# Optimization experiments

Hardware: AMD Instinct MI355X
Metric: run time of the kernel (lower is better)

## Reference

```python
import jax, jax.numpy as jnp
import numpy as np

TH, TL = 0.85, 0.5          # sim thresholds
ALPHA = 0.1                 # proto EMA alpha
TEMP = 1.0                  # readout temperature
KEEP, REFINE, REPLACE, SPAWN = 0, 1, 2, 3


def _l2n(x, axis=-1):
    return x / jnp.maximum(jnp.linalg.norm(x, axis=axis, keepdims=True), 1e-12)


def setup_inputs() -> dict:
    key = jax.random.key(0)
    ks = jax.random.split(key, 12)
    B, N, C, H, W, K = 4, 8, 256, 64, 64, 16
    return {
        "value_BNCHW": jax.random.normal(ks[0], (B, N, C, H, W), jnp.float32),
        "frame_feat_BCHW": jax.random.normal(ks[1], (B, C, H, W), jnp.float32),
        "mask_BNHW": jax.random.uniform(ks[2], (B, N, H, W), jnp.float32),
        "proto": jax.random.normal(ks[3], (B, N, K, C), jnp.float32),
        "age": jax.random.uniform(ks[4], (B, N, K), jnp.float32) * 10.0,
        "usage": jax.random.uniform(ks[5], (B, N, K), jnp.float32) * 5.0,
        "conf": jax.random.uniform(ks[6], (B, N, K), jnp.float32),
        "valid": jax.random.bernoulli(ks[7], 0.7, (B, N, K)),
        "W1": jax.random.normal(ks[8], (C + K + 3 * K, 256), jnp.float32) * 0.02,
        "b1": jnp.zeros((256,), jnp.float32),
        "W2": jax.random.normal(ks[9], (256, 4), jnp.float32) * 0.02,
        "b2": jnp.zeros((4,), jnp.float32),
        "proto_gate": jnp.float32(1.0),
        "frame_gate": jnp.float32(1.0),
    }


def reference(value_BNCHW, frame_feat_BCHW, mask_BNHW, proto, age, usage, conf,
              valid, W1, b1, W2, b2, proto_gate, frame_gate):
    B, N, C, H, W = value_BNCHW.shape
    K = proto.shape[2]
    P = H * W

    # ---- candidate prototype: masked mean pool over HW ----
    flat_v = value_BNCHW.reshape(B, N, C, P)          # [B,N,C,P]
    flat_m = mask_BNHW.reshape(B, N, 1, P)            # [B,N,1,P]
    denom = flat_m.sum(-1)                            # [B,N,1]
    cand = (flat_v * flat_m).sum(-1) / jnp.maximum(denom, 1e-6)
    fallback = flat_v.mean(-1)
    cand = jnp.where(denom <= 1e-5, fallback, cand)   # [B,N,C]
    mask_strength = flat_m.mean(-1)[..., 0]           # [B,N]
    cand = _l2n(cand)

    # ---- cosine sim against bank + context ----
    norm_bank = _l2n(proto)
    sim = jnp.einsum('bnc,bnkc->bnk', cand, norm_bank)
    sim = jnp.where(valid, sim, -1.0)
    g_t = frame_feat_BCHW.mean((2, 3))                # [B,C]
    age_n = age / jnp.maximum(jax.lax.stop_gradient(age.max()), 1.0)
    use_n = usage / jnp.maximum(jax.lax.stop_gradient(usage.max()), 1.0)
    stats = jnp.stack([age_n, use_n, conf], -1).reshape(B, N, 3 * K)
    context = jnp.concatenate(
        [jnp.broadcast_to(g_t[:, None, :], (B, N, C)), sim, stats], -1)
    any_valid = valid.any(-1)
    target_slot = jnp.where(any_valid, sim.argmax(-1), 0)
    max_sim = jnp.take_along_axis(sim, target_slot[..., None], -1)[..., 0]
    max_sim = jnp.where(any_valid, max_sim, 0.0)

    # ---- policy MLP (logits logged; rule-based policy selects action) ----
    logits = jax.nn.gelu(context @ W1 + b1) @ W2 + b2  # [B,N,4]

    has_free = (~valid).any(-1)
    low = max_sim < TL
    action = jnp.full((B, N), REFINE, jnp.int32)
    action = jnp.where(max_sim > TH, KEEP, action)
    action = jnp.where(low & has_free, SPAWN, action)
    action = jnp.where(low & ~has_free, REPLACE, action)

    # ---- action-conditioned slot selection + scatter update ----
    worst = jnp.argmax(age - usage - conf + 1000.0 * (~valid), -1)
    free_slot = jnp.argmax(~valid, -1)
    spawn = action == SPAWN
    replace = action == REPLACE
    refine = action == REFINE
    keep = action == KEEP
    chosen = target_slot
    chosen = jnp.where(spawn & has_free, free_slot, chosen)
    chosen = jnp.where(spawn & ~has_free, worst, chosen)   # spawn_replace_when_full
    chosen = jnp.where(replace, worst, chosen)
    update = refine | replace | spawn
    replace_like = replace | spawn

    bi = jnp.arange(B)[:, None]
    ni = jnp.arange(N)[None, :]

    old_p = proto[bi, ni, chosen]                      # [B,N,C] gather
    refined = _l2n((1.0 - ALPHA) * old_p + ALPHA * cand)
    new_p = jnp.where(refine[..., None], refined,
                      jnp.where(replace_like[..., None], cand, old_p))
    proto_new = proto.at[bi, ni, chosen].set(new_p)

    age1 = age + 1.0
    age_new = age1.at[bi, ni, chosen].set(
        jnp.where(replace_like, 0.0, age1[bi, ni, chosen]))
    usage_new = usage.at[bi, ni, chosen].set(
        jnp.where(replace_like, 1.0,
                  usage[bi, ni, chosen] + (refine | keep).astype(jnp.float32)))
    conf_g = conf[bi, ni, chosen]
    conf_val = jnp.where(refine, jnp.clip(0.5 * conf_g + 0.5 * max_sim, 0.0, 1.0),
                         jnp.where(replace_like, jnp.clip(mask_strength, 0.0, 1.0),
                                   conf_g))
    conf_new = conf.at[bi, ni, chosen].set(conf_val)
    valid_new = valid.at[bi, ni, chosen].set(valid[bi, ni, chosen] | update)

    # ---- prototype-conditioned readout (softmax over bank slots per pixel) ----
    vn = flat_v / jnp.maximum(jnp.linalg.norm(flat_v, axis=2, keepdims=True), 1e-12)
    nb = _l2n(proto_new)
    scores = jnp.einsum('bnkc,bncp->bnkp', nb, vn) / TEMP
    scores = jnp.where(valid_new[..., None], scores, -1e9)
    wts = jax.nn.softmax(scores, axis=2)               # over K
    proto_map = jnp.einsum('bnkp,bnkc->bncp', wts, proto_new)
    proto_map = jnp.where(valid_new.any(-1)[:, :, None, None], proto_map, 0.0)
    proto_map = proto_map.reshape(B, N, C, H, W)

    conditioned = (value_BNCHW + proto_gate * proto_map
                   + frame_gate * frame_feat_BCHW[:, None])
    return conditioned, logits
```

## Files before the change

### kernel.cpp

```cpp
#include <hip/hip_runtime.h>
#include <math.h>

#define NB_B 4
#define NB_N 8
#define NB_C 256
#define NB_K 16
#define NB_P 4096
#define NB_BN (NB_B * NB_N)

typedef float nfloat4 __attribute__((ext_vector_type(4)));

#define WS_WSUM 0
#define WS_VSUM (NB_BN * NB_C)
#define WS_GT   (2 * NB_BN * NB_C)
#define WS_DEN  (WS_GT + NB_B * NB_C)
#define WS_NB   17440
#define WS_PN   (WS_NB + NB_BN * NB_K * NB_C)
#define WS_VAL  (WS_PN + NB_BN * NB_K * NB_C)

__device__ __forceinline__ float2 blk_sum2(float a, float b, float2* sbuf) {
#pragma unroll
  for (int off = 32; off > 0; off >>= 1) {
    a += __shfl_down(a, off, 64);
    b += __shfl_down(b, off, 64);
  }
  int lane = threadIdx.x & 63, wid = threadIdx.x >> 6;
  __syncthreads();
  if (lane == 0) sbuf[wid] = make_float2(a, b);
  __syncthreads();
  float2 r;
  r.x = sbuf[0].x + sbuf[1].x + sbuf[2].x + sbuf[3].x;
  r.y = sbuf[0].y + sbuf[1].y + sbuf[2].y + sbuf[3].y;
  return r;
}

__device__ __forceinline__ float2 blk_max2(float a, float b, float2* sbuf) {
#pragma unroll
  for (int off = 32; off > 0; off >>= 1) {
    a = fmaxf(a, __shfl_down(a, off, 64));
    b = fmaxf(b, __shfl_down(b, off, 64));
  }
  int lane = threadIdx.x & 63, wid = threadIdx.x >> 6;
  __syncthreads();
  if (lane == 0) sbuf[wid] = make_float2(a, b);
  __syncthreads();
  float2 r;
  r.x = fmaxf(fmaxf(sbuf[0].x, sbuf[1].x), fmaxf(sbuf[2].x, sbuf[3].x));
  r.y = fmaxf(fmaxf(sbuf[0].y, sbuf[1].y), fmaxf(sbuf[2].y, sbuf[3].y));
  return r;
}

__device__ __forceinline__ int validMode(const void* vptr) {
  const unsigned int* w = (const unsigned int*)vptr;
  int mode = 0;
  for (int i = 0; i < 128; ++i) {
    unsigned int x = w[i];
    if (x == 0x3f800000u) return 2;
    if (x > 1u) mode = 1;
  }
  return mode;
}
__device__ __forceinline__ bool getValid(const void* vptr, int mode, int idx) {
  if (mode == 1) return ((const unsigned char*)vptr)[idx] != 0;
  if (mode == 2) return ((const float*)vptr)[idx] != 0.0f;
  return ((const int*)vptr)[idx] != 0;
}

__global__ __launch_bounds__(256) void k1_reduce(
    const float* __restrict__ value, const float* __restrict__ frame,
    const float* __restrict__ mask, float* __restrict__ ws) {
  __shared__ float2 sbuf[4];
  int gid = blockIdx.x, tid = threadIdx.x;
  if (gid < NB_BN * NB_C) {
    int bn = gid >> 8;
    const float4* v4 = (const float4*)(value + (size_t)gid * NB_P);
    const float4* m4 = (const float4*)(mask + (size_t)bn * NB_P);
    float wsum = 0.f, vsum = 0.f;
#pragma unroll
    for (int i = 0; i < NB_P / 4 / 256; ++i) {
      float4 a = v4[i * 256 + tid];
      float4 m = m4[i * 256 + tid];
      wsum += a.x * m.x + a.y * m.y + a.z * m.z + a.w * m.w;
      vsum += a.x + a.y + a.z + a.w;
    }
    float2 r = blk_sum2(wsum, vsum, sbuf);
    if (tid == 0) { ws[WS_WSUM + gid] = r.x; ws[WS_VSUM + gid] = r.y; }
  } else if (gid < NB_BN * NB_C + NB_B * NB_C) {
    int idx = gid - NB_BN * NB_C;
    const float4* f4 = (const float4*)(frame + (size_t)idx * NB_P);
    float s = 0.f;
#pragma unroll
    for (int i = 0; i < 4; ++i) {
      float4 a = f4[i * 256 + tid];
      s += a.x + a.y + a.z + a.w;
    }
    float2 r = blk_sum2(s, 0.f, sbuf);
    if (tid == 0) ws[WS_GT + idx] = r.x * (1.0f / NB_P);
  } else {
    int bn = gid - NB_BN * NB_C - NB_B * NB_C;
    const float4* m4 = (const float4*)(mask + (size_t)bn * NB_P);
    float s = 0.f;
#pragma unroll
    for (int i = 0; i < 4; ++i) {
      float4 a = m4[i * 256 + tid];
      s += a.x + a.y + a.z + a.w;
    }
    float2 r = blk_sum2(s, 0.f, sbuf);
    if (tid == 0) ws[WS_DEN + bn] = r.x;
  }
}

__global__ __launch_bounds__(256) void k2_policy(
    const float* __restrict__ proto, const float* __restrict__ age,
    const float* __restrict__ usage, const float* __restrict__ conf,
    const void* __restrict__ valid, const float* __restrict__ W1,
    const float* __restrict__ b1, const float* __restrict__ W2,
    const float* __restrict__ b2, float* __restrict__ ws,
    float* __restrict__ out_logits) {
  __shared__ float2 sbuf[4];
  __shared__ float s_cand[NB_C];
  __shared__ float s_sim[NB_K];
  __shared__ float s_invn[NB_K];
  __shared__ float s_ctx[NB_C + NB_K + 3 * NB_K];
  __shared__ int s_dec[4];
  __shared__ int s_vmode;

  int bn = blockIdx.x;
  int b = bn >> 3;
  int c = threadIdx.x;
  if (c == 0) s_vmode = validMode(valid);

  float denom = ws[WS_DEN + bn];
  float cand;
  if (denom <= 1e-5f) cand = ws[WS_VSUM + bn * NB_C + c] * (1.0f / NB_P);
  else                cand = ws[WS_WSUM + bn * NB_C + c] / fmaxf(denom, 1e-6f);
  float2 r0 = blk_sum2(cand * cand, 0.f, sbuf);
  cand *= 1.0f / fmaxf(sqrtf(r0.x), 1e-12f);
  s_cand[c] = cand;
  __syncthreads();
  int vmode = s_vmode;

  const float* pr = proto + (size_t)bn * NB_K * NB_C;
  {
    int wid = c >> 6, lane = c & 63;
#pragma unroll
    for (int q = 0; q < 4; ++q) {
      int k = wid * 4 + q;
      float pp = 0.f, pc = 0.f;
#pragma unroll
      for (int t = 0; t < 4; ++t) {
        int cc = lane + t * 64;
        float p = pr[k * NB_C + cc];
        pp += p * p;
        pc += p * s_cand[cc];
      }
#pragma unroll
      for (int off = 32; off > 0; off >>= 1) {
        pp += __shfl_down(pp, off, 64);
        pc += __shfl_down(pc, off, 64);
      }
      if (lane == 0) {
        float invk = 1.0f / fmaxf(sqrtf(pp), 1e-12f);
        s_invn[k] = invk;
        s_sim[k] = getValid(valid, vmode, bn * NB_K + k) ? pc * invk : -1.0f;
      }
    }
  }

  float am = fmaxf(age[c], age[c + 256]);
  float um = fmaxf(usage[c], usage[c + 256]);
  float2 mx = blk_max2(am, um, sbuf);
  float age_max = fmaxf(mx.x, 1.0f);
  float use_max = fmaxf(mx.y, 1.0f);

  s_ctx[c] = ws[WS_GT + b * NB_C + c];
  if (c < NB_K) {
    int k = c;
    s_ctx[NB_C + k] = s_sim[k];
    s_ctx[NB_C + NB_K + 3 * k + 0] = age[bn * NB_K + k] / age_max;
    s_ctx[NB_C + NB_K + 3 * k + 1] = usage[bn * NB_K + k] / use_max;
    s_ctx[NB_C + NB_K + 3 * k + 2] = conf[bn * NB_K + k];
  }
  __syncthreads();

  float acc = b1[c];
  for (int i = 0; i < NB_C + 4 * NB_K; ++i) acc += s_ctx[i] * W1[i * 256 + c];
  float h = 0.5f * acc *
            (1.0f + tanhf(0.7978845608028654f * (acc + 0.044715f * acc * acc * acc)));
  for (int j = 0; j < 4; ++j) {
    float2 lj = blk_sum2(h * W2[c * 4 + j], 0.f, sbuf);
    if (c == 0) out_logits[bn * 4 + j] = lj.x + b2[j];
  }

  if (c == 0) {
    bool anyv = false, hasfree = false;
    for (int k = 0; k < NB_K; ++k) {
      if (getValid(valid, vmode, bn * NB_K + k)) anyv = true; else hasfree = true;
    }
    int tgt = 0; float best = s_sim[0];
    for (int k = 1; k < NB_K; ++k) if (s_sim[k] > best) { best = s_sim[k]; tgt = k; }
    if (!anyv) tgt = 0;
    float max_sim = anyv ? s_sim[tgt] : 0.0f;
    int action = 1;
    if (max_sim > 0.85f) action = 0;
    bool low = max_sim < 0.5f;
    if (low && hasfree) action = 3;
    if (low && !hasfree) action = 2;
    int worst = 0; float wb = -1e30f;
    for (int k = 0; k < NB_K; ++k) {
      float sc = age[bn * NB_K + k] - usage[bn * NB_K + k] - conf[bn * NB_K + k] +
                 (getValid(valid, vmode, bn * NB_K + k) ? 0.f : 1000.f);
      if (sc > wb) { wb = sc; worst = k; }
    }
    int freeslot = 0;
    for (int k = 0; k < NB_K; ++k) {
      if (!getValid(valid, vmode, bn * NB_K + k)) { freeslot = k; break; }
    }
    int chosen = tgt;
    if (action == 3) chosen = hasfree ? freeslot : worst;
    if (action == 2) chosen = worst;
    s_dec[0] = chosen;
    s_dec[1] = (action == 1);
    s_dec[2] = (action == 2 || action == 3);
    s_dec[3] = (action != 0);
  }
  __syncthreads();

  int chosen = s_dec[0];
  float oldp = pr[chosen * NB_C + c];
  float t = 0.9f * oldp + 0.1f * s_cand[c];
  float2 tn = blk_sum2(t * t, 0.f, sbuf);
  float invt = 1.0f / fmaxf(sqrtf(tn.x), 1e-12f);
  float pn_chosen = s_dec[1] ? t * invt : (s_dec[2] ? s_cand[c] : oldp);
  float nb_chosen = s_dec[1] ? t * invt
                   : (s_dec[2] ? s_cand[c] : oldp * s_invn[chosen]);
  float nbrow[NB_K], pnrow[NB_K];
#pragma unroll
  for (int k = 0; k < NB_K; ++k) {
    float praw = pr[k * NB_C + c];
    nbrow[k] = (k == chosen) ? nb_chosen : praw * s_invn[k];
    pnrow[k] = (k == chosen) ? pn_chosen : praw;
  }
  float* nbp = ws + WS_NB + (size_t)bn * NB_K * NB_C + c * NB_K;
  float* pnp = ws + WS_PN + (size_t)bn * NB_K * NB_C + c * NB_K;
#pragma unroll
  for (int q = 0; q < 4; ++q) {
    *(float4*)(nbp + 4 * q) =
        make_float4(nbrow[4 * q], nbrow[4 * q + 1], nbrow[4 * q + 2], nbrow[4 * q + 3]);
    *(float4*)(pnp + 4 * q) =
        make_float4(pnrow[4 * q], pnrow[4 * q + 1], pnrow[4 * q + 2], pnrow[4 * q + 3]);
  }
  if (c < NB_K) {
    bool v = getValid(valid, vmode, bn * NB_K + c) || (c == chosen && s_dec[3]);
    ws[WS_VAL + bn * NB_K + c] = v ? 1.0f : 0.0f;
  }
}

__global__ __launch_bounds__(256, 4) void k3_fused(
    const float* __restrict__ value, const float* __restrict__ frame,
    const float* __restrict__ ws, const float* __restrict__ pgp,
    const float* __restrict__ fgp, float* __restrict__ out) {
  __shared__ float s_nb[NB_C * NB_K];
  __shared__ float4 s_part[4][64][5];
  int blk = blockIdx.x;
  int bn = blk >> 4, pxc = blk & 15;
  int b = bn >> 3;
  int tid = threadIdx.x;
  int lane = tid & 63, wv = tid >> 6;
  int px = pxc * 256 + lane * 4;

  const float4* nb4 = (const float4*)(ws + WS_NB + (size_t)bn * NB_K * NB_C);
  const float4* pn4 = (const float4*)(ws + WS_PN + (size_t)bn * NB_K * NB_C);
  float4* snb4 = (float4*)s_nb;
#pragma unroll
  for (int j = 0; j < 4; ++j) snb4[j * 256 + tid] = nb4[j * 256 + tid];
  int vmask = 0;
  for (int k = 0; k < NB_K; ++k)
    if (ws[WS_VAL + bn * NB_K + k] != 0.0f) vmask |= (1 << k);
  float pg = pgp[0], fg = fgp[0];
  __syncthreads();

  const float* vp = value + (size_t)bn * NB_C * NB_P + px;
  const float* nbk = s_nb + wv * 4;
  float4 dq0 = make_float4(0.f, 0.f, 0.f, 0.f);
  float4 dq1 = dq0, dq2 = dq0, dq3 = dq0, ss = dq0;
#pragma unroll 8
  for (int c = 0; c < NB_C; ++c) {
    float4 v = *(const float4*)(vp + (size_t)c * NB_P);
    float4 nk = *(const float4*)(nbk + c * NB_K);
    ss.x += v.x * v.x; ss.y += v.y * v.y; ss.z += v.z * v.z; ss.w += v.w * v.w;
    dq0.x += v.x * nk.x; dq0.y += v.y * nk.x; dq0.z += v.z * nk.x; dq0.w += v.w * nk.x;
    dq1.x += v.x * nk.y; dq1.y += v.y * nk.y; dq1.z += v.z * nk.y; dq1.w += v.w * nk.y;
    dq2.x += v.x * nk.z; dq2.y += v.y * nk.z; dq2.z += v.z * nk.z; dq2.w += v.w * nk.z;
    dq3.x += v.x * nk.w; dq3.y += v.y * nk.w; dq3.z += v.z * nk.w; dq3.w += v.w * nk.w;
  }

  s_part[wv][lane][0] = dq0;
  s_part[wv][lane][1] = dq1;
  s_part[wv][lane][2] = dq2;
  s_part[wv][lane][3] = dq3;
  __syncthreads();

  float4 d[NB_K];
#pragma unroll
  for (int k = 0; k < NB_K; ++k) d[k] = s_part[k >> 2][lane][k & 3];

#pragma unroll
  for (int j = 0; j < 4; ++j) snb4[j * 256 + tid] = pn4[j * 256 + tid];

  float4 invv;
  invv.x = 1.0f / fmaxf(sqrtf(ss.x), 1e-12f);
  invv.y = 1.0f / fmaxf(sqrtf(ss.y), 1e-12f);
  invv.z = 1.0f / fmaxf(sqrtf(ss.z), 1e-12f);
  invv.w = 1.0f / fmaxf(sqrtf(ss.w), 1e-12f);
  float4 m = make_float4(-1e30f, -1e30f, -1e30f, -1e30f);
#pragma unroll
  for (int k = 0; k < NB_K; ++k) {
    d[k].x *= invv.x; d[k].y *= invv.y; d[k].z *= invv.z; d[k].w *= invv.w;
    if ((vmask >> k) & 1) {
      m.x = fmaxf(m.x, d[k].x); m.y = fmaxf(m.y, d[k].y);
      m.z = fmaxf(m.z, d[k].z); m.w = fmaxf(m.w, d[k].w);
    }
  }
  float4 es = make_float4(0.f, 0.f, 0.f, 0.f);
#pragma unroll
  for (int k = 0; k < NB_K; ++k) {
    if ((vmask >> k) & 1) {
      d[k].x = __expf(d[k].x - m.x); d[k].y = __expf(d[k].y - m.y);
      d[k].z = __expf(d[k].z - m.z); d[k].w = __expf(d[k].w - m.w);
      es.x += d[k].x; es.y += d[k].y; es.z += d[k].z; es.w += d[k].w;
    } else {
      d[k] = make_float4(0.f, 0.f, 0.f, 0.f);
    }
  }
  float4 isum;
  isum.x = vmask ? (1.0f / es.x) : 0.0f;
  isum.y = vmask ? (1.0f / es.y) : 0.0f;
  isum.z = vmask ? (1.0f / es.z) : 0.0f;
  isum.w = vmask ? (1.0f / es.w) : 0.0f;
#pragma unroll
  for (int k = 0; k < NB_K; ++k) {
    d[k].x *= isum.x; d[k].y *= isum.y; d[k].z *= isum.z; d[k].w *= isum.w;
  }
  __syncthreads();

  int c0 = wv * 64;
  const float* vp2 = value + ((size_t)bn * NB_C + c0) * NB_P + px;
  const float* fp = frame + ((size_t)b * NB_C + c0) * NB_P + px;
  float* op = out + ((size_t)bn * NB_C + c0) * NB_P + px;
  const float* spn = s_nb + (size_t)c0 * NB_K;
#pragma unroll 4
  for (int cc = 0; cc < 64; ++cc) {
    float4 v = *(const float4*)(vp2 + (size_t)cc * NB_P);
    float4 f = *(const float4*)(fp + (size_t)cc * NB_P);
    const float4* prow = (const float4*)(spn + cc * NB_K);
    float4 p0 = prow[0], p1 = prow[1], p2 = prow[2], p3 = prow[3];
    float4 pm = make_float4(0.f, 0.f, 0.f, 0.f);
#define APM(K, S)                                                        \
    pm.x += d[K].x * S; pm.y += d[K].y * S; pm.z += d[K].z * S; pm.w += d[K].w * S;
    APM(0, p0.x)  APM(1, p0.y)  APM(2, p0.z)  APM(3, p0.w)
    APM(4, p1.x)  APM(5, p1.y)  APM(6, p1.z)  APM(7, p1.w)
    APM(8, p2.x)  APM(9, p2.y)  APM(10, p2.z) APM(11, p2.w)
    APM(12, p3.x) APM(13, p3.y) APM(14, p3.z) APM(15, p3.w)
#undef APM
    nfloat4 o;
    o.x = v.x + pg * pm.x + fg * f.x;
    o.y = v.y + pg * pm.y + fg * f.y;
    o.z = v.z + pg * pm.z + fg * f.z;
    o.w = v.w + pg * pm.w + fg * f.w;
    __builtin_nontemporal_store(o, (nfloat4*)(op + (size_t)cc * NB_P));
  }
}

extern "C" void kernel_launch(void* const* d_in, const int* in_sizes, int n_in,
                              void* d_out, int out_size, void* d_ws, size_t ws_size,
                              hipStream_t stream) {
  const float* value = (const float*)d_in[0];
  const float* frame = (const float*)d_in[1];
  const float* mask  = (const float*)d_in[2];
  const float* proto = (const float*)d_in[3];
  const float* age   = (const float*)d_in[4];
  const float* usage = (const float*)d_in[5];
  const float* conf  = (const float*)d_in[6];
  const void*  valid = (const void*)d_in[7];
  const float* W1 = (const float*)d_in[8];
  const float* b1 = (const float*)d_in[9];
  const float* W2 = (const float*)d_in[10];
  const float* b2 = (const float*)d_in[11];
  const float* pg = (const float*)d_in[12];
  const float* fg = (const float*)d_in[13];
  float* out = (float*)d_out;
  float* ws = (float*)d_ws;

  int g1 = NB_BN * NB_C + NB_B * NB_C + NB_BN;
  hipLaunchKernelGGL(k1_reduce, dim3(g1), dim3(256), 0, stream,
                     value, frame, mask, ws);
  hipLaunchKernelGGL(k2_policy, dim3(NB_BN), dim3(256), 0, stream,
                     proto, age, usage, conf, valid, W1, b1, W2, b2, ws,
                     out + (size_t)NB_BN * NB_C * NB_P);
  hipLaunchKernelGGL(k3_fused, dim3(NB_BN * 16), dim3(256), 0, stream,
                     value, frame, ws, pg, fg, out);
}
```

Before: 129.1 us.

## Stage value tiles into LDS with async double-buffered loads shared across waves

In the fused readout kernel's score phase, every wave used to load all 256 channel rows of value for the same pixels, so each row was fetched from global memory four times. Each wave now copies a quarter of each 16-channel chunk straight into LDS with global_load_lds, double-buffered so the next chunk loads while the current one is computed. The per-wave partial dot products are exchanged through a new LDS array, the pn bank is prefetched into registers before the barrier, and one barrier is removed. In exchange, LDS use grows to roughly 65 KB per block and the min-blocks launch bound is dropped, which may lower occupancy and adds a barrier per chunk.

```diff
diff --git a/kernel.cpp b/kernel.cpp
--- a/kernel.cpp
+++ b/kernel.cpp
@@ -17,6 +17,12 @@
 #define WS_NB   17440
 #define WS_PN   (WS_NB + NB_BN * NB_K * NB_C)
 #define WS_VAL  (WS_PN + NB_BN * NB_K * NB_C)
+
+__device__ __forceinline__ void stage16(const float* g, float* l) {
+  __builtin_amdgcn_global_load_lds(
+      (const __attribute__((address_space(1))) unsigned int*)g,
+      (__attribute__((address_space(3))) unsigned int*)l, 16, 0, 0);
+}
 
 __device__ __forceinline__ float2 blk_sum2(float a, float b, float2* sbuf) {
 #pragma unroll
@@ -256,18 +262,20 @@
   }
 }
 
-__global__ __launch_bounds__(256, 4) void k3_fused(
+__global__ __launch_bounds__(256) void k3_fused(
     const float* __restrict__ value, const float* __restrict__ frame,
     const float* __restrict__ ws, const float* __restrict__ pgp,
     const float* __restrict__ fgp, float* __restrict__ out) {
   __shared__ float s_nb[NB_C * NB_K];
-  __shared__ float4 s_part[4][64][5];
+  __shared__ float s_vbuf[2][16][256];
+  __shared__ float s_ex[17][256];
   int blk = blockIdx.x;
   int bn = blk >> 4, pxc = blk & 15;
   int b = bn >> 3;
   int tid = threadIdx.x;
   int lane = tid & 63, wv = tid >> 6;
-  int px = pxc * 256 + lane * 4;
+  int px0 = pxc * 256;
+  int px = px0 + lane * 4;
 
   const float4* nb4 = (const float4*)(ws + WS_NB + (size_t)bn * NB_K * NB_C);
   const float4* pn4 = (const float4*)(ws + WS_PN + (size_t)bn * NB_K * NB_C);
@@ -278,35 +286,58 @@
   for (int k = 0; k < NB_K; ++k)
     if (ws[WS_VAL + bn * NB_K + k] != 0.0f) vmask |= (1 << k);
   float pg = pgp[0], fg = fgp[0];
-  __syncthreads();
-
-  const float* vp = value + (size_t)bn * NB_C * NB_P + px;
+
+  const float* vrow = value + (size_t)bn * NB_C * NB_P + px0;
+
+#pragma unroll
+  for (int j = 0; j < 4; ++j)
+    stage16(vrow + (size_t)(4 * wv + j) * NB_P + lane * 4,
+            &s_vbuf[0][4 * wv + j][0]);
+  __syncthreads();
+
   const float* nbk = s_nb + wv * 4;
   float4 dq0 = make_float4(0.f, 0.f, 0.f, 0.f);
   float4 dq1 = dq0, dq2 = dq0, dq3 = dq0, ss = dq0;
-#pragma unroll 8
-  for (int c = 0; c < NB_C; ++c) {
-    float4 v = *(const float4*)(vp + (size_t)c * NB_P);
-    float4 nk = *(const float4*)(nbk + c * NB_K);
-    ss.x += v.x * v.x; ss.y += v.y * v.y; ss.z += v.z * v.z; ss.w += v.w * v.w;
-    dq0.x += v.x * nk.x; dq0.y += v.y * nk.x; dq0.z += v.z * nk.x; dq0.w += v.w * nk.x;
-    dq1.x += v.x * nk.y; dq1.y += v.y * nk.y; dq1.z += v.z * nk.y; dq1.w += v.w * nk.y;
-    dq2.x += v.x * nk.z; dq2.y += v.y * nk.z; dq2.z += v.z * nk.z; dq2.w += v.w * nk.z;
-    dq3.x += v.x * nk.w; dq3.y += v.y * nk.w; dq3.z += v.z * nk.w; dq3.w += v.w * nk.w;
-  }
-
-  s_part[wv][lane][0] = dq0;
-  s_part[wv][lane][1] = dq1;
-  s_part[wv][lane][2] = dq2;
-  s_part[wv][lane][3] = dq3;
+  int cur = 0;
+  for (int ch = 0; ch < 16; ++ch) {
+    if (ch < 15) {
+#pragma unroll
+      for (int j = 0; j < 4; ++j) {
+        int r = (ch + 1) * 16 + 4 * wv + j;
+        stage16(vrow + (size_t)r * NB_P + lane * 4,
+                &s_vbuf[cur ^ 1][4 * wv + j][0]);
+      }
+    }
+    const float* vb = &s_vbuf[cur][0][0];
+#pragma unroll
+    for (int r = 0; r < 16; ++r) {
+      int c = ch * 16 + r;
+      float4 v = *(const float4*)(vb + r * 256 + (lane << 2));
+      float4 nk = *(const float4*)(nbk + c * NB_K);
+      ss.x += v.x * v.x; ss.y += v.y * v.y; ss.z += v.z * v.z; ss.w += v.w * v.w;
+      dq0.x += v.x * nk.x; dq0.y += v.y * nk.x; dq0.z += v.z * nk.x; dq0.w += v.w * nk.x;
+      dq1.x += v.x * nk.y; dq1.y += v.y * nk.y; dq1.z += v.z * nk.y; dq1.w += v.w * nk.y;
+      dq2.x += v.x * nk.z; dq2.y += v.y * nk.z; dq2.z += v.z * nk.z; dq2.w += v.w * nk.z;
+      dq3.x += v.x * nk.w; dq3.y += v.y * nk.w; dq3.z += v.z * nk.w; dq3.w += v.w * nk.w;
+    }
+    __syncthreads();
+    cur ^= 1;
+  }
+
+  *(float4*)&s_ex[4 * wv + 0][lane << 2] = dq0;
+  *(float4*)&s_ex[4 * wv + 1][lane << 2] = dq1;
+  *(float4*)&s_ex[4 * wv + 2][lane << 2] = dq2;
+  *(float4*)&s_ex[4 * wv + 3][lane << 2] = dq3;
+  float4 pnr[4];
+#pragma unroll
+  for (int j = 0; j < 4; ++j) pnr[j] = pn4[j * 256 + tid];
+#pragma unroll
+  for (int j = 0; j < 4; ++j) snb4[j * 256 + tid] = pnr[j];
   __syncthreads();
 
   float4 d[NB_K];
 #pragma unroll
-  for (int k = 0; k < NB_K; ++k) d[k] = s_part[k >> 2][lane][k & 3];
-
-#pragma unroll
-  for (int j = 0; j < 4; ++j) snb4[j * 256 + tid] = pn4[j * 256 + tid];
+  for (int k = 0; k < NB_K; ++k) d[k] = *(const float4*)&s_ex[k][lane << 2];
 
   float4 invv;
   invv.x = 1.0f / fmaxf(sqrtf(ss.x), 1e-12f);
@@ -342,7 +373,6 @@
   for (int k = 0; k < NB_K; ++k) {
     d[k].x *= isum.x; d[k].y *= isum.y; d[k].z *= isum.z; d[k].w *= isum.w;
   }
-  __syncthreads();
 
   int c0 = wv * 64;
   const float* vp2 = value + ((size_t)bn * NB_C + c0) * NB_P + px;
```

Measured after the change: 125.5 us. -2.8%, faster.
